# Kernel tuning notes

Hardware: AMD Instinct MI355X
Metric: run time of the kernel (lower is better)

## Reference

```python
import jax, jax.numpy as jnp
import numpy as np

# ViT-Tiny + Performer attention (eval mode: dropout/droppath are no-ops)
B = 64
IMG, PATCH, GRID = 224, 16, 14
NPATCH, NTOK = 196, 197
EMBED, HEADS, HEAD_DIM = 192, 3, 64
DEPTH, FEAT, MLP, NCLS = 12, 256, 768, 1000
EXIT_IDXS = [4, 8, 12]
LN_EPS = 1e-5


def _ln(x, w, b):
    mu = x.mean(-1, keepdims=True)
    var = ((x - mu) ** 2).mean(-1, keepdims=True)
    return (x - mu) / jnp.sqrt(var + LN_EPS) * w + b


def setup_inputs() -> dict:
    key = jax.random.key(0)
    ks = jax.random.split(key, 16)
    n = lambda k, shape, s=0.02: jax.random.normal(k, shape, jnp.float32) * s
    inp = {}
    inp["x"] = jax.random.normal(ks[0], (B, 3, IMG, IMG), jnp.float32)
    inp["patch_w"] = n(ks[1], (EMBED, 3, PATCH, PATCH))
    inp["patch_b"] = jnp.zeros((EMBED,), jnp.float32)
    inp["pe_norm_w"] = jnp.ones((EMBED,), jnp.float32)
    inp["pe_norm_b"] = jnp.zeros((EMBED,), jnp.float32)
    inp["cls_token"] = n(ks[2], (1, 1, EMBED))
    inp["pos_embed"] = n(ks[3], (1, NTOK, EMBED))
    inp["norm1_w"] = jnp.ones((DEPTH, EMBED), jnp.float32)
    inp["norm1_b"] = jnp.zeros((DEPTH, EMBED), jnp.float32)
    inp["qkv_w"] = n(ks[4], (DEPTH, EMBED, 3 * EMBED))
    inp["qkv_b"] = jnp.zeros((DEPTH, 3 * EMBED), jnp.float32)
    # Gaussian random projection matrix (stands in for the orthogonal RF matrix)
    inp["proj_mat"] = jax.random.normal(ks[5], (DEPTH, FEAT, HEAD_DIM), jnp.float32)
    inp["attn_proj_w"] = n(ks[6], (DEPTH, EMBED, EMBED))
    inp["attn_proj_b"] = jnp.zeros((DEPTH, EMBED), jnp.float32)
    inp["norm2_w"] = jnp.ones((DEPTH, EMBED), jnp.float32)
    inp["norm2_b"] = jnp.zeros((DEPTH, EMBED), jnp.float32)
    inp["fc1_w"] = n(ks[7], (DEPTH, EMBED, MLP))
    inp["fc1_b"] = jnp.zeros((DEPTH, MLP), jnp.float32)
    inp["fc2_w"] = n(ks[8], (DEPTH, MLP, EMBED))
    inp["fc2_b"] = jnp.zeros((DEPTH, EMBED), jnp.float32)
    inp["exit_w"] = n(ks[9], (len(EXIT_IDXS), EMBED, NCLS))
    inp["exit_b"] = jnp.zeros((len(EXIT_IDXS), NCLS), jnp.float32)
    inp["final_norm_w"] = jnp.ones((EMBED,), jnp.float32)
    inp["final_norm_b"] = jnp.zeros((EMBED,), jnp.float32)
    inp["head_w"] = n(ks[10], (EMBED, NCLS))
    inp["head_b"] = jnp.zeros((NCLS,), jnp.float32)
    return inp


def _performer_attn(x, qw, qb, pm, pw, pb):
    Bn, N, C = x.shape
    qkv = (x @ qw + qb).reshape(Bn, N, 3, HEADS, HEAD_DIM).transpose(2, 0, 3, 1, 4)
    q, k, v = qkv[0], qkv[1], qkv[2]  # [B,H,N,d]

    def fmap(t):
        proj = jnp.einsum('bhnd,fd->bhnf', t, pm)  # random-feature projection
        norm_t = jnp.sum(t * t, axis=-1, keepdims=True) / 2.0
        return jnp.exp(proj - norm_t) * (HEAD_DIM ** -0.25)

    pq = fmap(q)  # [B,H,N,F]
    pk = fmap(k)
    k_cumsum = pk.sum(axis=2)  # [B,H,F]
    D_inv = 1.0 / jnp.einsum('bhnf,bhf->bhn', pq, k_cumsum)
    attn = jnp.einsum('bhnf,bhmf->bhnm', pq, pk)  # as in original (materializes NxN)
    out = jnp.einsum('bhnm,bhmd->bhnd', attn, v)
    out = out * D_inv[..., None]
    out = out.transpose(0, 2, 1, 3).reshape(Bn, N, C)
    return out @ pw + pb


def reference(x, patch_w, patch_b, pe_norm_w, pe_norm_b, cls_token, pos_embed,
              norm1_w, norm1_b, qkv_w, qkv_b, proj_mat, attn_proj_w, attn_proj_b,
              norm2_w, norm2_b, fc1_w, fc1_b, fc2_w, fc2_b,
              exit_w, exit_b, final_norm_w, final_norm_b, head_w, head_b):
    Bn = x.shape[0]
    # PatchEmbed: non-overlapping 16x16 conv == reshape + matmul (c,ph,pw order)
    p = x.reshape(Bn, 3, GRID, PATCH, GRID, PATCH).transpose(0, 2, 4, 1, 3, 5)
    p = p.reshape(Bn, NPATCH, 3 * PATCH * PATCH)
    tok = p @ patch_w.reshape(EMBED, -1).T + patch_b
    tok = _ln(tok, pe_norm_w, pe_norm_b)
    cls = jnp.broadcast_to(cls_token, (Bn, 1, EMBED))
    h = jnp.concatenate([cls, tok], axis=1) + pos_embed  # [B,197,192]

    exits = []
    for i in range(DEPTH):
        a = _performer_attn(_ln(h, norm1_w[i], norm1_b[i]), qkv_w[i], qkv_b[i],
                            proj_mat[i], attn_proj_w[i], attn_proj_b[i])
        h = h + a
        m = _ln(h, norm2_w[i], norm2_b[i])
        m = jax.nn.gelu(m @ fc1_w[i] + fc1_b[i], approximate=False) @ fc2_w[i] + fc2_b[i]
        h = h + m
        if (i + 1) in EXIT_IDXS:
            e = EXIT_IDXS.index(i + 1)
            z = h.mean(axis=1)  # AdaptiveAvgPool1d(1) over tokens
            exits.append(z @ exit_w[e] + exit_b[e])

    hf = _ln(h, final_norm_w, final_norm_b)
    logits = hf[:, 0] @ head_w + head_b  # cls-token head
    return (logits, exits[0], exits[1], exits[2])
```

## Files before the change

### kernel.cpp

```cpp
#include <hip/hip_runtime.h>
#include <math.h>

typedef unsigned short u16;
typedef unsigned int u32;
typedef __attribute__((ext_vector_type(8))) short short8;
typedef __attribute__((ext_vector_type(4))) float floatx4;

#define BB 64
#define NTOK 197
#define NPATCH 196
#define EMB 192
#define NH 3
#define HD 64
#define FEAT 256
#define MLPD 768
#define NCLS 1000
#define MTOT (BB*NTOK)
#define MPAT (BB*NPATCH)
#define BHT (BB*NH)

__device__ __forceinline__ u16 f2bf(float x) {
    u32 u = __builtin_bit_cast(u32, x);
    u32 r = u + 0x7FFFu + ((u >> 16) & 1u);
    return (u16)(r >> 16);
}
__device__ __forceinline__ float bf2f(u16 u) {
    return __builtin_bit_cast(float, (u32)u << 16);
}
__device__ __forceinline__ float sqr8bf(uint4 v) {
    float s = 0.f;
    float t;
    t = bf2f((u16)(v.x & 0xffff)); s += t*t;  t = bf2f((u16)(v.x >> 16)); s += t*t;
    t = bf2f((u16)(v.y & 0xffff)); s += t*t;  t = bf2f((u16)(v.y >> 16)); s += t*t;
    t = bf2f((u16)(v.z & 0xffff)); s += t*t;  t = bf2f((u16)(v.z >> 16)); s += t*t;
    t = bf2f((u16)(v.w & 0xffff)); s += t*t;  t = bf2f((u16)(v.w >> 16)); s += t*t;
    return s;
}

__global__ void cvt_bf16(const float* __restrict__ in, u16* __restrict__ out, int n)
{
    const int i = blockIdx.x * 256 + threadIdx.x;
    if (i < n) out[i] = f2bf(in[i]);
}

__global__ void tr_bf16_t(const float* __restrict__ in, u16* __restrict__ out,
                          int R, int C)
{
    __shared__ u16 t[32][33];
    const int l = blockIdx.z;
    const int c0 = blockIdx.x * 32, r0 = blockIdx.y * 32;
    const int tx = threadIdx.x & 31, ty = threadIdx.x >> 5;
    const float* ip = in + ((size_t)l * R + r0) * C + c0;
#pragma unroll
    for (int j = 0; j < 4; ++j)
        t[ty + j*8][tx] = f2bf(ip[(size_t)(ty + j*8) * C + tx]);
    __syncthreads();
    u16* op = out + ((size_t)l * C + c0) * R + r0;
#pragma unroll
    for (int j = 0; j < 4; ++j)
        op[(size_t)(ty + j*8) * R + tx] = t[tx][ty + j*8];
}

__global__ void tr_bf16_g(const float* __restrict__ in, u16* __restrict__ out,
                          int R, int C)
{
    __shared__ u16 t[32][33];
    const int l = blockIdx.z;
    const int c0 = blockIdx.x * 32, r0 = blockIdx.y * 32;
    const int tx = threadIdx.x & 31, ty = threadIdx.x >> 5;
    const float* ip = in + (size_t)l * R * C;
#pragma unroll
    for (int j = 0; j < 4; ++j) {
        const int r = r0 + ty + j*8, c = c0 + tx;
        t[ty + j*8][tx] = (r < R && c < C) ? f2bf(ip[(size_t)r * C + c]) : (u16)0;
    }
    __syncthreads();
    u16* op = out + (size_t)l * C * R;
#pragma unroll
    for (int j = 0; j < 4; ++j) {
        const int c = c0 + ty + j*8, r = r0 + tx;
        if (c < C && r < R)
            op[(size_t)c * R + r] = t[tx][ty + j*8];
    }
}

__global__ __launch_bounds__(256) void gemm_bf16(
    const u16* __restrict__ A, const u16* __restrict__ Bt,
    const float* __restrict__ bias,
    float* __restrict__ Cf, u16* __restrict__ Cb,
    int M, int N, int K, int mode, int ntx)
{
    __shared__ u16 As[128][72];
    __shared__ u16 Bs[64][72];
    const int tid = threadIdx.x;
    const int lane = tid & 63, wave = tid >> 6;
    const int l16 = lane & 15, quad = lane >> 4;
    const int nwg = gridDim.x;
    const int q = nwg >> 3, r = nwg & 7;
    const int xcd = blockIdx.x & 7, jj = blockIdx.x >> 3;
    const int wg = (xcd < r ? xcd * (q + 1) : r * (q + 1) + (xcd - r) * q) + jj;
    const int m0 = (wg / ntx) * 128, n0 = (wg % ntx) * 64;
    const int arow = tid >> 1, aof = (tid & 1) * 32;
    const int brow = tid >> 2, bof = (tid & 3) * 16;

    floatx4 acc[2][4];
#pragma unroll
    for (int i = 0; i < 2; ++i)
#pragma unroll
        for (int j = 0; j < 4; ++j) acc[i][j] = (floatx4){0.f,0.f,0.f,0.f};

    const int gmA = m0 + arow;
    const bool aok = (gmA < M);
    const u16* ap = A + (size_t)gmA * K + aof;
    const u16* bp = Bt + (size_t)(n0 + brow) * K + bof;

    for (int k0 = 0; k0 < K; k0 += 64) {
        uint4 a0 = {0,0,0,0}, a1 = {0,0,0,0}, a2 = {0,0,0,0}, a3 = {0,0,0,0};
        if (aok) {
            a0 = *(const uint4*)(ap + k0);
            a1 = *(const uint4*)(ap + k0 + 8);
            a2 = *(const uint4*)(ap + k0 + 16);
            a3 = *(const uint4*)(ap + k0 + 24);
        }
        const uint4 b0 = *(const uint4*)(bp + k0);
        const uint4 b1 = *(const uint4*)(bp + k0 + 8);
        if (k0) __syncthreads();
        *(uint4*)&As[arow][aof]      = a0;
        *(uint4*)&As[arow][aof + 8]  = a1;
        *(uint4*)&As[arow][aof + 16] = a2;
        *(uint4*)&As[arow][aof + 24] = a3;
        *(uint4*)&Bs[brow][bof]      = b0;
        *(uint4*)&Bs[brow][bof + 8]  = b1;
        __syncthreads();
#pragma unroll
        for (int ks = 0; ks < 2; ++ks) {
            short8 af[2], bf[4];
#pragma unroll
            for (int rf = 0; rf < 2; ++rf)
                af[rf] = *(const short8*)&As[wave*32 + rf*16 + l16][ks*32 + quad*8];
#pragma unroll
            for (int cf = 0; cf < 4; ++cf)
                bf[cf] = *(const short8*)&Bs[cf*16 + l16][ks*32 + quad*8];
#pragma unroll
            for (int rf = 0; rf < 2; ++rf)
#pragma unroll
                for (int cf = 0; cf < 4; ++cf)
                    acc[rf][cf] = __builtin_amdgcn_mfma_f32_16x16x32_bf16(af[rf], bf[cf], acc[rf][cf], 0, 0, 0);
        }
    }

    if (mode == 0) {
        const int rbase = m0 + wave * 32 + quad * 4;
        const int cbase = n0 + l16;
#pragma unroll
        for (int rf = 0; rf < 2; ++rf) {
#pragma unroll
            for (int reg = 0; reg < 4; ++reg) {
                const int gm = rbase + rf * 16 + reg;
                if (gm >= M) continue;
#pragma unroll
                for (int cf = 0; cf < 4; ++cf) {
                    const int gn = cbase + cf * 16;
                    Cf[(size_t)gm * N + gn] = acc[rf][cf][reg] + bias[gn];
                }
            }
        }
        return;
    }

    __syncthreads();
#pragma unroll
    for (int rf = 0; rf < 2; ++rf) {
#pragma unroll
        for (int cf = 0; cf < 4; ++cf) {
            const int lc = cf * 16 + l16;
            const float bia = bias[n0 + lc];
#pragma unroll
            for (int reg = 0; reg < 4; ++reg) {
                const int lr = wave * 32 + rf * 16 + quad * 4 + reg;
                float v = acc[rf][cf][reg] + bia;
                if (mode == 2)
                    v = 0.5f * v * (1.f + erff(v * 0.70710678118654752f));
                const int phys = (((lc >> 3) ^ (lr & 7)) << 3) | (lc & 7);
                As[lr][phys] = f2bf(v);
            }
        }
    }
    __syncthreads();
#pragma unroll
    for (int it = 0; it < 4; ++it) {
        const int idx = it * 256 + tid;
        const int row = idx >> 3, c8 = idx & 7;
        const int pc8 = c8 ^ (row & 7);
        const uint4 val = *(const uint4*)&As[row][pc8 * 8];
        const int gm = m0 + row;
        if (gm < M)
            *(uint4*)&Cb[(size_t)gm * N + n0 + c8 * 8] = val;
    }
}

__global__ __launch_bounds__(256) void gemm_ln(
    const u16* __restrict__ A, const u16* __restrict__ Bt,
    const float* __restrict__ bias,
    const float* __restrict__ lnw, const float* __restrict__ lnb,
    float* __restrict__ H, u16* __restrict__ outb, int K)
{
    __shared__ u16 As[32][72];
    __shared__ u16 Bs[192][72];
    __shared__ float red_s[2][32][2];
    const int tid = threadIdx.x;
    const int lane = tid & 63, wave = tid >> 6;
    const int wr = wave & 1;
    const int wc = wave >> 1;
    const int l16 = lane & 15, quad = lane >> 4;
    const int m0 = blockIdx.x * 32;
    const int srowA = tid >> 3, skofA = (tid & 7) * 8;
    const int srow = tid >> 2, skof = (tid & 3) * 16;

    floatx4 acc[6];
#pragma unroll
    for (int j = 0; j < 6; ++j) acc[j] = (floatx4){0.f,0.f,0.f,0.f};

    const u16* ap = A + (size_t)(m0 + srowA) * K + skofA;
    const u16* bp = Bt + (size_t)srow * K + skof;
    const size_t bstep = (size_t)64 * K;

    for (int k0 = 0; k0 < K; k0 += 64) {
        const uint4 a0 = *(const uint4*)(ap + k0);
        const uint4 b0 = *(const uint4*)(bp + k0);
        const uint4 b1 = *(const uint4*)(bp + k0 + 8);
        const uint4 b2 = *(const uint4*)(bp + bstep + k0);
        const uint4 b3 = *(const uint4*)(bp + bstep + k0 + 8);
        const uint4 b4 = *(const uint4*)(bp + 2*bstep + k0);
        const uint4 b5 = *(const uint4*)(bp + 2*bstep + k0 + 8);
        if (k0) __syncthreads();
        *(uint4*)&As[srowA][skofA]         = a0;
        *(uint4*)&Bs[srow][skof]           = b0;
        *(uint4*)&Bs[srow][skof + 8]       = b1;
        *(uint4*)&Bs[srow + 64][skof]      = b2;
        *(uint4*)&Bs[srow + 64][skof + 8]  = b3;
        *(uint4*)&Bs[srow + 128][skof]     = b4;
        *(uint4*)&Bs[srow + 128][skof + 8] = b5;
        __syncthreads();
#pragma unroll
        for (int ks = 0; ks < 2; ++ks) {
            const short8 af = *(const short8*)&As[wr*16 + l16][ks*32 + quad*8];
            short8 bf[6];
#pragma unroll
            for (int cf = 0; cf < 6; ++cf)
                bf[cf] = *(const short8*)&Bs[wc*96 + cf*16 + l16][ks*32 + quad*8];
#pragma unroll
            for (int cf = 0; cf < 6; ++cf)
                acc[cf] = __builtin_amdgcn_mfma_f32_16x16x32_bf16(af, bf[cf], acc[cf], 0, 0, 0);
        }
    }

    float s_[4], q_[4];
#pragma unroll
    for (int reg = 0; reg < 4; ++reg) { s_[reg] = 0.f; q_[reg] = 0.f; }

#pragma unroll
    for (int cf = 0; cf < 6; ++cf) {
        const int gn = wc * 96 + cf * 16 + l16;
        const float bia = bias[gn];
#pragma unroll
        for (int reg = 0; reg < 4; ++reg) {
            const int gm = m0 + wr * 16 + quad * 4 + reg;
            float v = acc[cf][reg] + bia + H[(size_t)gm * EMB + gn];
            H[(size_t)gm * EMB + gn] = v;
            acc[cf][reg] = v;
            s_[reg] += v;
            q_[reg] += v * v;
        }
    }

    if (lnw) {
#pragma unroll
        for (int reg = 0; reg < 4; ++reg) {
            float s = s_[reg], q = q_[reg];
            s += __shfl_xor(s, 1); q += __shfl_xor(q, 1);
            s += __shfl_xor(s, 2); q += __shfl_xor(q, 2);
            s += __shfl_xor(s, 4); q += __shfl_xor(q, 4);
            s += __shfl_xor(s, 8); q += __shfl_xor(q, 8);
            if (l16 == 0) {
                const int rl = wr * 16 + quad * 4 + reg;
                red_s[wc][rl][0] = s;
                red_s[wc][rl][1] = q;
            }
        }
        __syncthreads();
#pragma unroll
        for (int reg = 0; reg < 4; ++reg) {
            const int rl = wr * 16 + quad * 4 + reg;
            const float ts = red_s[0][rl][0] + red_s[1][rl][0];
            const float tq = red_s[0][rl][1] + red_s[1][rl][1];
            const float mu = ts * (1.f / 192.f);
            const float var = tq * (1.f / 192.f) - mu * mu;
            const float rstd = rsqrtf(fmaxf(var, 0.f) + 1e-5f);
            const int gm = m0 + rl;
#pragma unroll
            for (int cf = 0; cf < 6; ++cf) {
                const int gn = wc * 96 + cf * 16 + l16;
                const float y = (acc[cf][reg] - mu) * rstd * lnw[gn] + lnb[gn];
                outb[(size_t)gm * EMB + gn] = f2bf(y);
            }
        }
    }
}

__global__ __launch_bounds__(256) void mlp_ln(
    const u16* __restrict__ A, const u16* __restrict__ W1t,
    const float* __restrict__ b1,
    const u16* __restrict__ W2t, const float* __restrict__ b2,
    const float* __restrict__ lnw, const float* __restrict__ lnb,
    float* __restrict__ H, u16* __restrict__ outb)
{
    __shared__ u16 As[32][200];
    __shared__ u16 W1s[64][200];
    __shared__ u16 W2s[192][72];
    __shared__ u16 Ms[32][72];
    __shared__ float red_s[4][32][2];
    const int tid = threadIdx.x;
    const int lane = tid & 63, wave = tid >> 6;
    const int l16 = lane & 15, quad = lane >> 4;
    const int m0 = blockIdx.x * 32;

    {
        const int row = tid >> 3, cb = (tid & 7) * 24;
        const u16* ap = A + (size_t)(m0 + row) * EMB + cb;
#pragma unroll
        for (int j = 0; j < 3; ++j)
            *(uint4*)&As[row][cb + j * 8] = *(const uint4*)(ap + j * 8);
    }
    __syncthreads();
    short8 af[2][6];
#pragma unroll
    for (int rf = 0; rf < 2; ++rf)
#pragma unroll
        for (int ks = 0; ks < 6; ++ks)
            af[rf][ks] = *(const short8*)&As[rf*16 + l16][ks*32 + quad*8];

    floatx4 acc[2][3];
#pragma unroll
    for (int i = 0; i < 2; ++i)
#pragma unroll
        for (int j = 0; j < 3; ++j) acc[i][j] = (floatx4){0.f,0.f,0.f,0.f};

    for (int c = 0; c < 12; ++c) {
        if (c) __syncthreads();
        {
            const int row = tid >> 2, cb = (tid & 3) * 48;
            const u16* wp = W1t + (size_t)(c * 64 + row) * EMB + cb;
#pragma unroll
            for (int j = 0; j < 6; ++j)
                *(uint4*)&W1s[row][cb + j * 8] = *(const uint4*)(wp + j * 8);
        }
#pragma unroll
        for (int j = 0; j < 6; ++j) {
            const int idx = j * 256 + tid;
            const int e = idx >> 3, o = (idx & 7) * 8;
            *(uint4*)&W2s[e][o] = *(const uint4*)(W2t + (size_t)e * MLPD + c * 64 + o);
        }
        __syncthreads();

        floatx4 mf[2] = {(floatx4){0.f,0.f,0.f,0.f}, (floatx4){0.f,0.f,0.f,0.f}};
#pragma unroll
        for (int ks = 0; ks < 6; ++ks) {
            const short8 w1f = *(const short8*)&W1s[wave*16 + l16][ks*32 + quad*8];
            mf[0] = __builtin_amdgcn_mfma_f32_16x16x32_bf16(af[0][ks], w1f, mf[0], 0, 0, 0);
            mf[1] = __builtin_amdgcn_mfma_f32_16x16x32_bf16(af[1][ks], w1f, mf[1], 0, 0, 0);
        }
        const float bia = b1[c * 64 + wave * 16 + l16];
#pragma unroll
        for (int rf = 0; rf < 2; ++rf)
#pragma unroll
            for (int reg = 0; reg < 4; ++reg) {
                float v = mf[rf][reg] + bia;
                v = 0.5f * v * (1.f + erff(v * 0.70710678118654752f));
                Ms[rf*16 + quad*4 + reg][wave*16 + l16] = f2bf(v);
            }
        __syncthreads();

#pragma unroll
        for (int ks2 = 0; ks2 < 2; ++ks2) {
            short8 a2[2], w2f[3];
#pragma unroll
            for (int rf = 0; rf < 2; ++rf)
                a2[rf] = *(const short8*)&Ms[rf*16 + l16][ks2*32 + quad*8];
#pragma unroll
            for (int cf = 0; cf < 3; ++cf)
                w2f[cf] = *(const short8*)&W2s[wave*48 + cf*16 + l16][ks2*32 + quad*8];
#pragma unroll
            for (int rf = 0; rf < 2; ++rf)
#pragma unroll
                for (int cf = 0; cf < 3; ++cf)
                    acc[rf][cf] = __builtin_amdgcn_mfma_f32_16x16x32_bf16(a2[rf], w2f[cf], acc[rf][cf], 0, 0, 0);
        }
    }

    float s_[2][4], q_[2][4];
#pragma unroll
    for (int rf = 0; rf < 2; ++rf)
#pragma unroll
        for (int reg = 0; reg < 4; ++reg) { s_[rf][reg] = 0.f; q_[rf][reg] = 0.f; }

#pragma unroll
    for (int rf = 0; rf < 2; ++rf) {
#pragma unroll
        for (int cf = 0; cf < 3; ++cf) {
            const int gn = wave * 48 + cf * 16 + l16;
            const float bia = b2[gn];
#pragma unroll
            for (int reg = 0; reg < 4; ++reg) {
                const int gm = m0 + rf * 16 + quad * 4 + reg;
                float v = acc[rf][cf][reg] + bia + H[(size_t)gm * EMB + gn];
                H[(size_t)gm * EMB + gn] = v;
                acc[rf][cf][reg] = v;
                s_[rf][reg] += v;
                q_[rf][reg] += v * v;
            }
        }
    }

    if (lnw) {
#pragma unroll
        for (int rf = 0; rf < 2; ++rf)
#pragma unroll
            for (int reg = 0; reg < 4; ++reg) {
                float s = s_[rf][reg], q = q_[rf][reg];
                s += __shfl_xor(s, 1); q += __shfl_xor(q, 1);
                s += __shfl_xor(s, 2); q += __shfl_xor(q, 2);
                s += __shfl_xor(s, 4); q += __shfl_xor(q, 4);
                s += __shfl_xor(s, 8); q += __shfl_xor(q, 8);
                if (l16 == 0) {
                    const int rl = rf * 16 + quad * 4 + reg;
                    red_s[wave][rl][0] = s;
                    red_s[wave][rl][1] = q;
                }
            }
        __syncthreads();
#pragma unroll
        for (int rf = 0; rf < 2; ++rf) {
#pragma unroll
            for (int reg = 0; reg < 4; ++reg) {
                const int rl = rf * 16 + quad * 4 + reg;
                const float ts = red_s[0][rl][0] + red_s[1][rl][0]
                               + red_s[2][rl][0] + red_s[3][rl][0];
                const float tq = red_s[0][rl][1] + red_s[1][rl][1]
                               + red_s[2][rl][1] + red_s[3][rl][1];
                const float mu = ts * (1.f / 192.f);
                const float var = tq * (1.f / 192.f) - mu * mu;
                const float rstd = rsqrtf(fmaxf(var, 0.f) + 1e-5f);
                const int gm = m0 + rl;
#pragma unroll
                for (int cf = 0; cf < 3; ++cf) {
                    const int gn = wave * 48 + cf * 16 + l16;
                    const float y = (acc[rf][cf][reg] - mu) * rstd * lnw[gn] + lnb[gn];
                    outb[(size_t)gm * EMB + gn] = f2bf(y);
                }
            }
        }
    }
}

__global__ __launch_bounds__(256) void attn_pkv(
    const u16* __restrict__ qkv, const u16* __restrict__ pmb,
    u16* __restrict__ kvT, float* __restrict__ ksum)
{
    __shared__ u16 pm_s[64][72];
    __shared__ u16 kt_s[64][72];
    __shared__ u16 vT_s[64][72];
    __shared__ u16 pkT_s[64][72];
    __shared__ float nrm_s[64];
    __shared__ float ksum_s[64];

    const int tid = threadIdx.x;
    const int lane = tid & 63, wave = tid >> 6;
    const int l16 = lane & 15, quad = lane >> 4;
    const int fq = blockIdx.x, bh = blockIdx.y, b = bh / NH, h = bh % NH;
    const int fwave = wave * 16;
    const int srow = tid >> 2, skof = (tid & 3) * 16;
    const float scale = 0.35355339059327373f;

#pragma unroll
    for (int j = 0; j < 2; ++j) {
        const int flat = j * 256 + tid;
        const int row = flat >> 3, o = (flat & 7) * 8;
        *(uint4*)&pm_s[row][o] = *(const uint4*)(pmb + (size_t)(fq * 64 + row) * 64 + o);
    }
    if (tid < 64) ksum_s[tid] = 0.f;

    floatx4 kv[4];
#pragma unroll
    for (int i = 0; i < 4; ++i) kv[i] = (floatx4){0.f,0.f,0.f,0.f};

    uint4 k0v = {0,0,0,0}, k1v = {0,0,0,0}, v0v = {0,0,0,0}, v1v = {0,0,0,0};
    {
        const u16* kp = qkv + ((size_t)(b * NTOK + srow)) * 576 + 192 + h * 64 + skof;
        k0v = *(const uint4*)kp; k1v = *(const uint4*)(kp + 8);
        v0v = *(const uint4*)(kp + 192); v1v = *(const uint4*)(kp + 200);
    }

    for (int t = 0; t < 4; ++t) {
        const int ncur = t * 64 + srow;
        if (t) __syncthreads();
        *(uint4*)&kt_s[srow][skof]     = k0v;
        *(uint4*)&kt_s[srow][skof + 8] = k1v;
        {
            u16 vv[16];
            vv[0]=(u16)(v0v.x&0xffff);  vv[1]=(u16)(v0v.x>>16);
            vv[2]=(u16)(v0v.y&0xffff);  vv[3]=(u16)(v0v.y>>16);
            vv[4]=(u16)(v0v.z&0xffff);  vv[5]=(u16)(v0v.z>>16);
            vv[6]=(u16)(v0v.w&0xffff);  vv[7]=(u16)(v0v.w>>16);
            vv[8]=(u16)(v1v.x&0xffff);  vv[9]=(u16)(v1v.x>>16);
            vv[10]=(u16)(v1v.y&0xffff); vv[11]=(u16)(v1v.y>>16);
            vv[12]=(u16)(v1v.z&0xffff); vv[13]=(u16)(v1v.z>>16);
            vv[14]=(u16)(v1v.w&0xffff); vv[15]=(u16)(v1v.w>>16);
#pragma unroll
            for (int j = 0; j < 16; ++j) vT_s[skof + j][srow] = vv[j];
        }
        float sq = sqr8bf(k0v) + sqr8bf(k1v);
        sq += __shfl_xor(sq, 1);
        sq += __shfl_xor(sq, 2);
        if ((tid & 3) == 0) nrm_s[srow] = (ncur < NTOK) ? 0.5f * sq : 1e30f;
        __syncthreads();

        if (t < 3) {
            const int n = (t + 1) * 64 + srow;
            k0v = (uint4){0,0,0,0}; k1v = (uint4){0,0,0,0};
            v0v = (uint4){0,0,0,0}; v1v = (uint4){0,0,0,0};
            if (n < NTOK) {
                const u16* kp = qkv + ((size_t)(b * NTOK + n)) * 576 + 192 + h * 64 + skof;
                k0v = *(const uint4*)kp; k1v = *(const uint4*)(kp + 8);
                v0v = *(const uint4*)(kp + 192); v1v = *(const uint4*)(kp + 200);
            }
        }

        floatx4 pa[4];
#pragma unroll
        for (int i = 0; i < 4; ++i) pa[i] = (floatx4){0.f,0.f,0.f,0.f};
#pragma unroll
        for (int ks = 0; ks < 2; ++ks) {
            const short8 bpm = *(const short8*)&pm_s[fwave + l16][ks*32 + quad*8];
#pragma unroll
            for (int rf = 0; rf < 4; ++rf) {
                const short8 a = *(const short8*)&kt_s[rf*16 + l16][ks*32 + quad*8];
                pa[rf] = __builtin_amdgcn_mfma_f32_16x16x32_bf16(a, bpm, pa[rf], 0, 0, 0);
            }
        }

        float ksp = 0.f;
        const int floc = fwave + l16;
#pragma unroll
        for (int rf = 0; rf < 4; ++rf) {
            const int nl = rf * 16 + quad * 4;
            const u16 b0 = f2bf(__expf(pa[rf][0] - nrm_s[nl + 0]) * scale);
            const u16 b1 = f2bf(__expf(pa[rf][1] - nrm_s[nl + 1]) * scale);
            const u16 b2 = f2bf(__expf(pa[rf][2] - nrm_s[nl + 2]) * scale);
            const u16 b3 = f2bf(__expf(pa[rf][3] - nrm_s[nl + 3]) * scale);
            ksp += bf2f(b0) + bf2f(b1) + bf2f(b2) + bf2f(b3);
            *(u32*)&pkT_s[floc][nl]     = (u32)b0 | ((u32)b1 << 16);
            *(u32*)&pkT_s[floc][nl + 2] = (u32)b2 | ((u32)b3 << 16);
        }
        {
            float v = ksp;
            v += __shfl_xor(v, 16);
            v += __shfl_xor(v, 32);
            if (quad == 0) ksum_s[floc] += v;
        }

#pragma unroll
        for (int ks = 0; ks < 2; ++ks) {
            const short8 bpk = *(const short8*)&pkT_s[fwave + l16][ks*32 + quad*8];
#pragma unroll
            for (int rf = 0; rf < 4; ++rf) {
                const short8 a = *(const short8*)&vT_s[rf*16 + l16][ks*32 + quad*8];
                kv[rf] = __builtin_amdgcn_mfma_f32_16x16x32_bf16(a, bpk, kv[rf], 0, 0, 0);
            }
        }
    }

    __syncthreads();
    if (tid < 64) ksum[(size_t)bh * 256 + fq * 64 + tid] = ksum_s[tid];
    const int fg = fq * 64 + fwave + l16;
#pragma unroll
    for (int rf = 0; rf < 4; ++rf) {
#pragma unroll
        for (int reg = 0; reg < 4; ++reg) {
            const int d = rf * 16 + quad * 4 + reg;
            kvT[((size_t)bh * 64 + d) * 256 + fg] = f2bf(kv[rf][reg]);
        }
    }
}

__global__ __launch_bounds__(256) void attn_out(
    const u16* __restrict__ qkv, const u16* __restrict__ pmb,
    const u16* __restrict__ kvT, const float* __restrict__ ksum,
    u16* __restrict__ attn_o)
{
    __shared__ u16 pm_s[256][72];
    __shared__ u16 q_s[64][72];
    __shared__ u16 pq_s[64][264];
    __shared__ u16 kv_s[64][264];
    __shared__ float nrm_s[64];
    __shared__ float den_s[4][64];

    const int tid = threadIdx.x;
    const int lane = tid & 63, wave = tid >> 6;
    const int l16 = lane & 15, quad = lane >> 4;
    const int bh = blockIdx.y, b = bh / NH, h = bh % NH;
    const int n0 = blockIdx.x * 64;
    const int fbase = wave * 64;
    const int srow = tid >> 2, skof = (tid & 3) * 16;
    const float scale = 0.35355339059327373f;

#pragma unroll
    for (int j = 0; j < 8; ++j) {
        const int flat = j * 256 + tid;
        const int f = flat >> 3, o = (flat & 7) * 8;
        *(uint4*)&pm_s[f][o] = *(const uint4*)(pmb + f * 64 + o);
    }
#pragma unroll
    for (int j = 0; j < 8; ++j) {
        const int flat = j * 256 + tid;
        const int d = flat >> 5, o = (flat & 31) * 8;
        *(uint4*)&kv_s[d][o] = *(const uint4*)(kvT + ((size_t)bh * 64 + d) * 256 + o);
    }
    {
        const int n = n0 + srow;
        uint4 q0 = {0,0,0,0}, q1 = {0,0,0,0};
        if (n < NTOK) {
            const u16* qp = qkv + ((size_t)(b * NTOK + n)) * 576 + h * 64 + skof;
            q0 = *(const uint4*)qp; q1 = *(const uint4*)(qp + 8);
        }
        *(uint4*)&q_s[srow][skof]     = q0;
        *(uint4*)&q_s[srow][skof + 8] = q1;
        float sq = sqr8bf(q0) + sqr8bf(q1);
        sq += __shfl_xor(sq, 1);
        sq += __shfl_xor(sq, 2);
        if ((tid & 3) == 0) nrm_s[srow] = (n < NTOK) ? 0.5f * sq : 1e30f;
    }
    float ksr[4];
#pragma unroll
    for (int cf = 0; cf < 4; ++cf)
        ksr[cf] = ksum[(size_t)bh * 256 + fbase + cf * 16 + l16];
    __syncthreads();

    floatx4 pa[4][4];
#pragma unroll
    for (int i = 0; i < 4; ++i)
#pragma unroll
        for (int j = 0; j < 4; ++j) pa[i][j] = (floatx4){0.f,0.f,0.f,0.f};
#pragma unroll
    for (int ks = 0; ks < 2; ++ks) {
        short8 a[4], bb[4];
#pragma unroll
        for (int rf = 0; rf < 4; ++rf)
            a[rf] = *(const short8*)&q_s[rf*16 + l16][ks*32 + quad*8];
#pragma unroll
        for (int cf = 0; cf < 4; ++cf)
            bb[cf] = *(const short8*)&pm_s[fbase + cf*16 + l16][ks*32 + quad*8];
#pragma unroll
        for (int rf = 0; rf < 4; ++rf)
#pragma unroll
            for (int cf = 0; cf < 4; ++cf)
                pa[rf][cf] = __builtin_amdgcn_mfma_f32_16x16x32_bf16(a[rf], bb[cf], pa[rf][cf], 0, 0, 0);
    }

    float dpart[16];
#pragma unroll
    for (int i = 0; i < 16; ++i) dpart[i] = 0.f;
#pragma unroll
    for (int rf = 0; rf < 4; ++rf) {
        const int nl = rf * 16 + quad * 4;
        const float nr0 = nrm_s[nl + 0], nr1 = nrm_s[nl + 1];
        const float nr2 = nrm_s[nl + 2], nr3 = nrm_s[nl + 3];
#pragma unroll
        for (int cf = 0; cf < 4; ++cf) {
            const int f = fbase + cf * 16 + l16;
            const u16 b0 = f2bf(__expf(pa[rf][cf][0] - nr0) * scale);
            const u16 b1 = f2bf(__expf(pa[rf][cf][1] - nr1) * scale);
            const u16 b2 = f2bf(__expf(pa[rf][cf][2] - nr2) * scale);
            const u16 b3 = f2bf(__expf(pa[rf][cf][3] - nr3) * scale);
            pq_s[nl + 0][f] = b0;
            pq_s[nl + 1][f] = b1;
            pq_s[nl + 2][f] = b2;
            pq_s[nl + 3][f] = b3;
            dpart[rf*4 + 0] += bf2f(b0) * ksr[cf];
            dpart[rf*4 + 1] += bf2f(b1) * ksr[cf];
            dpart[rf*4 + 2] += bf2f(b2) * ksr[cf];
            dpart[rf*4 + 3] += bf2f(b3) * ksr[cf];
        }
    }
#pragma unroll
    for (int i = 0; i < 16; ++i) {
        float d = dpart[i];
        d += __shfl_xor(d, 1); d += __shfl_xor(d, 2);
        d += __shfl_xor(d, 4); d += __shfl_xor(d, 8);
        dpart[i] = d;
    }
    if (l16 == 0) {
#pragma unroll
        for (int rf = 0; rf < 4; ++rf)
#pragma unroll
            for (int reg = 0; reg < 4; ++reg)
                den_s[wave][rf*16 + quad*4 + reg] = dpart[rf*4 + reg];
    }
    __syncthreads();

    const int wr = wave & 1, wc = wave >> 1;
    floatx4 oc[2][2];
#pragma unroll
    for (int i = 0; i < 2; ++i)
#pragma unroll
        for (int j = 0; j < 2; ++j) oc[i][j] = (floatx4){0.f,0.f,0.f,0.f};
#pragma unroll
    for (int ks = 0; ks < 8; ++ks) {
        short8 a[2], bb[2];
#pragma unroll
        for (int rf = 0; rf < 2; ++rf)
            a[rf] = *(const short8*)&pq_s[wr*32 + rf*16 + l16][ks*32 + quad*8];
#pragma unroll
        for (int cf = 0; cf < 2; ++cf)
            bb[cf] = *(const short8*)&kv_s[wc*32 + cf*16 + l16][ks*32 + quad*8];
#pragma unroll
        for (int rf = 0; rf < 2; ++rf)
#pragma unroll
            for (int cf = 0; cf < 2; ++cf)
                oc[rf][cf] = __builtin_amdgcn_mfma_f32_16x16x32_bf16(a[rf], bb[cf], oc[rf][cf], 0, 0, 0);
    }

#pragma unroll
    for (int rf = 0; rf < 2; ++rf) {
#pragma unroll
        for (int reg = 0; reg < 4; ++reg) {
            const int nl = wr*32 + rf*16 + quad*4 + reg;
            const int gn = n0 + nl;
            if (gn >= NTOK) continue;
            const float di = 1.f / (den_s[0][nl] + den_s[1][nl] + den_s[2][nl] + den_s[3][nl]);
#pragma unroll
            for (int cf = 0; cf < 2; ++cf) {
                const int d = wc*32 + cf*16 + l16;
                attn_o[((size_t)(b * NTOK + gn)) * EMB + h * 64 + d] =
                    f2bf(oc[rf][cf][reg] * di);
            }
        }
    }
}

__global__ void im2col_kernel(const float* __restrict__ x, u16* __restrict__ p, int total)
{
    const int i = blockIdx.x * 256 + threadIdx.x;
    if (i >= total) return;
    const int col = i % 768, row = i / 768;
    const int px = col & 15, py = (col >> 4) & 15, c = col >> 8;
    const int gx = row % 14, gy = (row / 14) % 14, b = row / 196;
    p[i] = f2bf(x[((size_t)(b * 3 + c) * 224 + gy * 16 + py) * 224 + gx * 16 + px]);
}

__global__ void embed_finish(const float* __restrict__ tok, const float* __restrict__ cls,
                             const float* __restrict__ pos, const float* __restrict__ w,
                             const float* __restrict__ b,
                             const float* __restrict__ n1w, const float* __restrict__ n1b,
                             float* __restrict__ h, u16* __restrict__ outb)
{
    const int wid = threadIdx.x >> 6, lane = threadIdx.x & 63;
    const int r = blockIdx.x * 4 + wid;
    if (r >= MTOT) return;
    const int bb = r / NTOK, t = r % NTOK;
    float y0, y1, y2;
    if (t == 0) {
        y0 = cls[lane]       + pos[lane];
        y1 = cls[lane + 64]  + pos[lane + 64];
        y2 = cls[lane + 128] + pos[lane + 128];
    } else {
        const float* p = tok + ((size_t)bb * NPATCH + (t - 1)) * EMB;
        float x0 = p[lane], x1 = p[lane + 64], x2 = p[lane + 128];
        float s = x0 + x1 + x2;
#pragma unroll
        for (int off = 32; off; off >>= 1) s += __shfl_xor(s, off);
        const float mu = s * (1.f / 192.f);
        const float d0 = x0 - mu, d1 = x1 - mu, d2 = x2 - mu;
        float v = d0 * d0 + d1 * d1 + d2 * d2;
#pragma unroll
        for (int off = 32; off; off >>= 1) v += __shfl_xor(v, off);
        const float rstd = rsqrtf(v * (1.f / 192.f) + 1e-5f);
        const float* pr = pos + (size_t)t * EMB;
        y0 = d0 * rstd * w[lane]       + b[lane]       + pr[lane];
        y1 = d1 * rstd * w[lane + 64]  + b[lane + 64]  + pr[lane + 64];
        y2 = d2 * rstd * w[lane + 128] + b[lane + 128] + pr[lane + 128];
    }
    float* q = h + (size_t)r * EMB;
    q[lane] = y0; q[lane + 64] = y1; q[lane + 128] = y2;
    float s2 = y0 + y1 + y2;
#pragma unroll
    for (int off = 32; off; off >>= 1) s2 += __shfl_xor(s2, off);
    const float mu2 = s2 * (1.f / 192.f);
    const float e0 = y0 - mu2, e1 = y1 - mu2, e2 = y2 - mu2;
    float v2 = e0 * e0 + e1 * e1 + e2 * e2;
#pragma unroll
    for (int off = 32; off; off >>= 1) v2 += __shfl_xor(v2, off);
    const float rstd2 = rsqrtf(v2 * (1.f / 192.f) + 1e-5f);
    u16* o = outb + (size_t)r * EMB;
    o[lane]       = f2bf(e0 * rstd2 * n1w[lane]       + n1b[lane]);
    o[lane + 64]  = f2bf(e1 * rstd2 * n1w[lane + 64]  + n1b[lane + 64]);
    o[lane + 128] = f2bf(e2 * rstd2 * n1w[lane + 128] + n1b[lane + 128]);
}

__global__ void ln192(const float* __restrict__ in, int in_stride,
                      const float* __restrict__ w, const float* __restrict__ b,
                      u16* __restrict__ outb, float* __restrict__ outf, int rows)
{
    const int wid = threadIdx.x >> 6, lane = threadIdx.x & 63;
    const int r = blockIdx.x * 4 + wid;
    if (r >= rows) return;
    const float* p = in + (size_t)r * in_stride;
    float x0 = p[lane], x1 = p[lane + 64], x2 = p[lane + 128];
    float s = x0 + x1 + x2;
#pragma unroll
    for (int off = 32; off; off >>= 1) s += __shfl_xor(s, off);
    const float mu = s * (1.f / 192.f);
    const float d0 = x0 - mu, d1 = x1 - mu, d2 = x2 - mu;
    float v = d0 * d0 + d1 * d1 + d2 * d2;
#pragma unroll
    for (int off = 32; off; off >>= 1) v += __shfl_xor(v, off);
    const float rstd = rsqrtf(v * (1.f / 192.f) + 1e-5f);
    const float y0 = d0 * rstd * w[lane]       + b[lane];
    const float y1 = d1 * rstd * w[lane + 64]  + b[lane + 64];
    const float y2 = d2 * rstd * w[lane + 128] + b[lane + 128];
    if (outf) {
        float* q = outf + (size_t)r * EMB;
        q[lane] = y0; q[lane + 64] = y1; q[lane + 128] = y2;
    } else {
        u16* q = outb + (size_t)r * EMB;
        q[lane] = f2bf(y0); q[lane + 64] = f2bf(y1); q[lane + 128] = f2bf(y2);
    }
}

__global__ __launch_bounds__(256) void gemm_cls(
    const u16* __restrict__ A, const u16* __restrict__ Bt,
    const float* __restrict__ bias, float* __restrict__ C,
    int N, int K)
{
    __shared__ u16 As[64][72];
    __shared__ u16 Bs[64][72];
    const int tid = threadIdx.x;
    const int lane = tid & 63, wave = tid >> 6;
    const int wr = wave & 1, wc = wave >> 1;
    const int l16 = lane & 15, quad = lane >> 4;
    const int n0 = blockIdx.x * 64;
    const int srow = tid >> 2, skof = (tid & 3) * 16;

    floatx4 acc[2][2];
#pragma unroll
    for (int i = 0; i < 2; ++i)
#pragma unroll
        for (int j = 0; j < 2; ++j) acc[i][j] = (floatx4){0.f,0.f,0.f,0.f};

    const u16* ap = A + (size_t)srow * K + skof;
    int brow_g = n0 + srow;  if (brow_g > N - 1) brow_g = N - 1;
    const u16* bp = Bt + (size_t)brow_g * K + skof;

    for (int k0 = 0; k0 < K; k0 += 64) {
        const uint4 a0 = *(const uint4*)(ap + k0);
        const uint4 a1 = *(const uint4*)(ap + k0 + 8);
        const uint4 b0 = *(const uint4*)(bp + k0);
        const uint4 b1 = *(const uint4*)(bp + k0 + 8);
        if (k0) __syncthreads();
        *(uint4*)&As[srow][skof]     = a0;
        *(uint4*)&As[srow][skof + 8] = a1;
        *(uint4*)&Bs[srow][skof]     = b0;
        *(uint4*)&Bs[srow][skof + 8] = b1;
        __syncthreads();
#pragma unroll
        for (int ks = 0; ks < 2; ++ks) {
            short8 af[2], bf[2];
#pragma unroll
            for (int rf = 0; rf < 2; ++rf)
                af[rf] = *(const short8*)&As[wr*32 + rf*16 + l16][ks*32 + quad*8];
#pragma unroll
            for (int cf = 0; cf < 2; ++cf)
                bf[cf] = *(const short8*)&Bs[wc*32 + cf*16 + l16][ks*32 + quad*8];
#pragma unroll
            for (int rf = 0; rf < 2; ++rf)
#pragma unroll
                for (int cf = 0; cf < 2; ++cf)
                    acc[rf][cf] = __builtin_amdgcn_mfma_f32_16x16x32_bf16(af[rf], bf[cf], acc[rf][cf], 0, 0, 0);
        }
    }

#pragma unroll
    for (int rf = 0; rf < 2; ++rf) {
#pragma unroll
        for (int reg = 0; reg < 4; ++reg) {
            const int gm = wr*32 + rf*16 + quad*4 + reg;
#pragma unroll
            for (int cf = 0; cf < 2; ++cf) {
                const int gn = n0 + wc*32 + cf*16 + l16;
                if (gn < N)
                    C[(size_t)gm * N + gn] = acc[rf][cf][reg] + bias[gn];
            }
        }
    }
}

__global__ void pool_kernel(const float* __restrict__ h, u16* __restrict__ pooled)
{
    __shared__ float red[192];
    const int b = blockIdx.x;
    const int slice = threadIdx.x / 192;
    const int e = threadIdx.x % 192;
    float s = 0.f;
    for (int n = slice; n < NTOK; n += 2)
        s += h[((size_t)(b * NTOK + n)) * EMB + e];
    if (slice == 1) red[e] = s;
    __syncthreads();
    if (slice == 0)
        pooled[b * EMB + e] = f2bf((s + red[e]) * (1.f / 197.f));
}

extern "C" void kernel_launch(void* const* d_in, const int* in_sizes, int n_in,
                              void* d_out, int out_size, void* d_ws, size_t ws_size,
                              hipStream_t stream)
{
    const float* x          = (const float*)d_in[0];
    const float* patch_w    = (const float*)d_in[1];
    const float* patch_b    = (const float*)d_in[2];
    const float* pe_norm_w  = (const float*)d_in[3];
    const float* pe_norm_b  = (const float*)d_in[4];
    const float* cls_token  = (const float*)d_in[5];
    const float* pos_embed  = (const float*)d_in[6];
    const float* norm1_w    = (const float*)d_in[7];
    const float* norm1_b    = (const float*)d_in[8];
    const float* qkv_w      = (const float*)d_in[9];
    const float* qkv_b      = (const float*)d_in[10];
    const float* proj_mat   = (const float*)d_in[11];
    const float* attn_pw    = (const float*)d_in[12];
    const float* attn_pb    = (const float*)d_in[13];
    const float* norm2_w    = (const float*)d_in[14];
    const float* norm2_b    = (const float*)d_in[15];
    const float* fc1_w      = (const float*)d_in[16];
    const float* fc1_b      = (const float*)d_in[17];
    const float* fc2_w      = (const float*)d_in[18];
    const float* fc2_b      = (const float*)d_in[19];
    const float* exit_w     = (const float*)d_in[20];
    const float* exit_b     = (const float*)d_in[21];
    const float* fnorm_w    = (const float*)d_in[22];
    const float* fnorm_b    = (const float*)d_in[23];
    const float* head_w     = (const float*)d_in[24];
    const float* head_b     = (const float*)d_in[25];
    float* out = (float*)d_out;

    float* ws = (float*)d_ws;
    float* H     = ws + 0;
    u16*   QKVB  = (u16*)(ws + 2420736);
    u16*   XLNB  = (u16*)(ws + 6051840);
    u16*   EXWT  = (u16*)(ws + 7262208);
    u16*   HWT   = (u16*)(ws + 7550208);
    u16*   POOLB = (u16*)(ws + 7646208);
    u16*   KVT   = (u16*)(ws + 19968000);
    u16*   MIDB  = (u16*)(ws + 21540864);
    u16*   ATNB  = (u16*)(ws + 26382336);
    float* KSUM  = ws + 27617280;
    u16*   QKVWT = (u16*)(ws + 27666432);
    u16*   APWT  = (u16*)(ws + 28329984);
    u16*   F1WT  = (u16*)(ws + 28551168);
    u16*   F2WT  = (u16*)(ws + 29435904);
    u16*   PATWB = (u16*)(ws + 30320640);
    u16*   PMB   = (u16*)(ws + 30394368);
    u16*   P_IMB = MIDB;
    float* TOK   = (float*)QKVB;

    if (ws_size < (size_t)30492672 * sizeof(float)) return;

    cvt_bf16<<<(147456 + 255) / 256, 256, 0, stream>>>(patch_w, PATWB, 147456);
    cvt_bf16<<<(196608 + 255) / 256, 256, 0, stream>>>(proj_mat, PMB, 196608);
    tr_bf16_t<<<dim3(18, 6, 12), 256, 0, stream>>>(qkv_w,   QKVWT, 192, 576);
    tr_bf16_t<<<dim3(6, 6, 12),  256, 0, stream>>>(attn_pw, APWT,  192, 192);
    tr_bf16_t<<<dim3(24, 6, 12), 256, 0, stream>>>(fc1_w,   F1WT,  192, 768);
    tr_bf16_t<<<dim3(6, 24, 12), 256, 0, stream>>>(fc2_w,   F2WT,  768, 192);
    tr_bf16_g<<<dim3(32, 6, 3), 256, 0, stream>>>(exit_w, EXWT, 192, 1000);
    tr_bf16_g<<<dim3(32, 6, 1), 256, 0, stream>>>(head_w, HWT,  192, 1000);

    im2col_kernel<<<(MPAT * 768 + 255) / 256, 256, 0, stream>>>(x, P_IMB, MPAT * 768);
    gemm_bf16<<<294, 256, 0, stream>>>(P_IMB, PATWB, patch_b,
                                       TOK, nullptr, MPAT, EMB, 768, 0, 3);
    embed_finish<<<(MTOT + 3) / 4, 256, 0, stream>>>(TOK, cls_token, pos_embed,
                                                     pe_norm_w, pe_norm_b,
                                                     norm1_w, norm1_b, H, XLNB);

    for (int i = 0; i < 12; ++i) {
        const u16* qwt  = QKVWT + (size_t)i * 576 * 192;
        const u16* pwt  = APWT  + (size_t)i * 192 * 192;
        const u16* f1wt = F1WT  + (size_t)i * 768 * 192;
        const u16* f2wt = F2WT  + (size_t)i * 192 * 768;
        const u16* pmb  = PMB   + (size_t)i * 256 * 64;
        const float* qb  = qkv_b   + (size_t)i * 576;
        const float* pb  = attn_pb + (size_t)i * 192;
        const float* f1b = fc1_b   + (size_t)i * 768;

        gemm_bf16<<<891, 256, 0, stream>>>(XLNB, qwt, qb,
                                           nullptr, QKVB, MTOT, 576, 192, 3, 9);
        attn_pkv<<<dim3(4, BHT), 256, 0, stream>>>(QKVB, pmb, KVT, KSUM);
        attn_out<<<dim3(4, BHT), 256, 0, stream>>>(QKVB, pmb, KVT, KSUM, ATNB);
        gemm_ln<<<394, 256, 0, stream>>>(ATNB, pwt, pb,
                                         norm2_w + (size_t)i * EMB, norm2_b + (size_t)i * EMB,
                                         H, XLNB, EMB);
        const float* nw = (i < 11) ? norm1_w + (size_t)(i + 1) * EMB : nullptr;
        const float* nb = (i < 11) ? norm1_b + (size_t)(i + 1) * EMB : nullptr;
        mlp_ln<<<394, 256, 0, stream>>>(XLNB, f1wt, f1b, f2wt,
                                        fc2_b + (size_t)i * 192, nw, nb, H, XLNB);

        const int e = (i == 3) ? 0 : (i == 7) ? 1 : (i == 11) ? 2 : -1;
        if (e >= 0) {
            pool_kernel<<<BB, 384, 0, stream>>>(H, POOLB);
            gemm_cls<<<16, 256, 0, stream>>>(POOLB, EXWT + (size_t)e * 1000 * 192,
                                             exit_b + (size_t)e * 1000,
                                             out + (size_t)(1 + e) * BB * NCLS,
                                             NCLS, EMB);
        }
    }

    ln192<<<(BB + 3) / 4, 256, 0, stream>>>(H, NTOK * EMB, fnorm_w, fnorm_b,
                                            XLNB, nullptr, BB);
    gemm_cls<<<16, 256, 0, stream>>>(XLNB, HWT, head_b, out, NCLS, EMB);
}
```

Measured before the change: 1.366 ms.

## Add dedicated 64x64-tile QKV GEMM kernel with XCD-aware block remapping

```diff
diff --git a/kernel.cpp b/kernel.cpp
--- a/kernel.cpp
+++ b/kernel.cpp
@@ -196,6 +196,70 @@
         const int gm = m0 + row;
         if (gm < M)
             *(uint4*)&Cb[(size_t)gm * N + n0 + c8 * 8] = val;
+    }
+}
+
+__global__ __launch_bounds__(256) void gemm_qkv(
+    const u16* __restrict__ A, const u16* __restrict__ Bt,
+    const float* __restrict__ bias, u16* __restrict__ Cb)
+{
+    __shared__ u16 As[64][200];
+    __shared__ u16 Bs[64][200];
+    const int tid = threadIdx.x;
+    const int lane = tid & 63, wave = tid >> 6;
+    const int l16 = lane & 15, quad = lane >> 4;
+    const int nwg = gridDim.x;
+    const int q = nwg >> 3, r = nwg & 7;
+    const int xcd = blockIdx.x & 7, jj = blockIdx.x >> 3;
+    const int wg = (xcd < r ? xcd * (q + 1) : r * (q + 1) + (xcd - r) * q) + jj;
+    const int m0 = (wg / 9) * 64, n0 = (wg % 9) * 64;
+    const int srow = tid >> 2, skof = (tid & 3) * 48;
+
+    const u16* ap = A + (size_t)(m0 + srow) * EMB + skof;
+    const u16* bp = Bt + (size_t)(n0 + srow) * EMB + skof;
+#pragma unroll
+    for (int j = 0; j < 6; ++j)
+        *(uint4*)&As[srow][skof + j * 8] = *(const uint4*)(ap + j * 8);
+#pragma unroll
+    for (int j = 0; j < 6; ++j)
+        *(uint4*)&Bs[srow][skof + j * 8] = *(const uint4*)(bp + j * 8);
+    __syncthreads();
+
+    floatx4 acc[4];
+#pragma unroll
+    for (int j = 0; j < 4; ++j) acc[j] = (floatx4){0.f,0.f,0.f,0.f};
+#pragma unroll
+    for (int ks = 0; ks < 6; ++ks) {
+        const short8 af = *(const short8*)&As[wave*16 + l16][ks*32 + quad*8];
+        short8 bf[4];
+#pragma unroll
+        for (int cf = 0; cf < 4; ++cf)
+            bf[cf] = *(const short8*)&Bs[cf*16 + l16][ks*32 + quad*8];
+#pragma unroll
+        for (int cf = 0; cf < 4; ++cf)
+            acc[cf] = __builtin_amdgcn_mfma_f32_16x16x32_bf16(af, bf[cf], acc[cf], 0, 0, 0);
+    }
+
+    __syncthreads();
+#pragma unroll
+    for (int cf = 0; cf < 4; ++cf) {
+        const int lc = cf * 16 + l16;
+        const float bia = bias[n0 + lc];
+#pragma unroll
+        for (int reg = 0; reg < 4; ++reg) {
+            const int lr = wave * 16 + quad * 4 + reg;
+            const int phys = (((lc >> 3) ^ (lr & 7)) << 3) | (lc & 7);
+            As[lr][phys] = f2bf(acc[cf][reg] + bia);
+        }
+    }
+    __syncthreads();
+#pragma unroll
+    for (int it = 0; it < 2; ++it) {
+        const int idx = it * 256 + tid;
+        const int row = idx >> 3, c8 = idx & 7;
+        const int pc8 = c8 ^ (row & 7);
+        const uint4 val = *(const uint4*)&As[row][pc8 * 8];
+        *(uint4*)&Cb[(size_t)(m0 + row) * 576 + n0 + c8 * 8] = val;
     }
 }
 
@@ -999,8 +1063,7 @@
         const float* pb  = attn_pb + (size_t)i * 192;
         const float* f1b = fc1_b   + (size_t)i * 768;
 
-        gemm_bf16<<<891, 256, 0, stream>>>(XLNB, qwt, qb,
-                                           nullptr, QKVB, MTOT, 576, 192, 3, 9);
+        gemm_qkv<<<1773, 256, 0, stream>>>(XLNB, qwt, qb, QKVB);
         attn_pkv<<<dim3(4, BHT), 256, 0, stream>>>(QKVB, pmb, KVT, KSUM);
         attn_out<<<dim3(4, BHT), 256, 0, stream>>>(QKVB, pmb, KVT, KSUM, ATNB);
         gemm_ln<<<394, 256, 0, stream>>>(ATNB, pwt, pb,
```

New measurement: 1.355 ms. No clear change (-0.7%).
